# Performance work log

Hardware: AMD Instinct MI355X
Metric: run time of the kernel (lower is better)

## Reference

```python
import jax, jax.numpy as jnp
import numpy as np

B, T, E = 4, 2048, 1024
H, D = 8, 128  # num_query_heads, head_dimension (single shared KV head -> MQA)


def sinusoidal_pe(length, dim, dtype=jnp.float32):
    """Standard additive sinusoidal PE table of shape (length, dim)."""
    pos = jnp.arange(length, dtype=jnp.float32)[:, None]            # (L, 1)
    inv_freq = jnp.exp(-jnp.log(jnp.float32(10000.0)) * (jnp.arange(0, dim, 2, dtype=jnp.float32) / dim))
    ang = pos * inv_freq[None, :]                                    # (L, dim//2)
    pe = jnp.zeros((length, dim), dtype=jnp.float32)
    pe = pe.at[:, 0::2].set(jnp.sin(ang)).at[:, 1::2].set(jnp.cos(ang))
    return pe.astype(dtype)


def setup_inputs() -> dict:
    key = jax.random.key(0)
    kx, kq, kk, kv, ko = jax.random.split(key, 5)
    s = 0.02  # weight init scale
    return {
        "x": jax.random.normal(kx, (B, T, E), dtype=jnp.float32),
        "Wq": jax.random.normal(kq, (H * D, E), dtype=jnp.float32) * s,
        "Wk": jax.random.normal(kk, (D, E), dtype=jnp.float32) * s,
        "Wv": jax.random.normal(kv, (D, E), dtype=jnp.float32) * s,
        "Wo": jax.random.normal(ko, (E, H * D), dtype=jnp.float32) * s,
    }


def reference(x, Wq, Wk, Wv, Wo):
    Bv, Tv, Ev = x.shape
    scale = 1.0 / jnp.sqrt(jnp.float32(D)).astype(x.dtype)

    q = (x @ Wq.T).reshape(Bv, Tv, H, D)        # (B, T, H, D)
    k = (x @ Wk.T).reshape(Bv, Tv, 1, D)        # (B, T, 1, D) single KV head
    v = (x @ Wv.T).reshape(Bv, Tv, 1, D)

    # positional_embedding applied along axis -2 (as in (.., seq, dim) layout):
    # for k (B,T,1,D) the -2 axis has length 1 -> adds pe[0];
    # for q after permute (B,H,T,D) the -2 axis is T -> full table.
    k = k + sinusoidal_pe(1, D, k.dtype)        # broadcast over (B, T)

    q = jnp.transpose(q, (0, 2, 1, 3))          # (B, H, T, D)
    k1 = k[:, :, 0, :]                          # (B, T, D) shared KV head
    v1 = v[:, :, 0, :]                          # (B, T, D)

    q = q + sinusoidal_pe(Tv, D, q.dtype)[None, None]

    # MQA SDPA: broadcast single K/V head across H query heads
    scores = jnp.einsum("bhtd,bsd->bhts", q, k1) * scale   # (B, H, T, T)
    causal = jnp.tril(jnp.ones((Tv, Tv), dtype=bool))
    scores = jnp.where(causal[None, None], scores, jnp.finfo(scores.dtype).min)
    probs = jax.nn.softmax(scores, axis=-1)
    attn = jnp.einsum("bhts,bsd->bhtd", probs, v1)          # (B, H, T, D)

    out = jnp.transpose(attn, (0, 2, 1, 3)).reshape(Bv, Tv, H * D)
    return out @ Wo.T                                        # (B, T, E)
```

## Files before the change

### kernel.cpp

```cpp
#include <hip/hip_runtime.h>
#include <hip/hip_bf16.h>
#include <cstdint>
#include <cstddef>

#define B_ 4
#define T_ 2048
#define E_ 1024
#define H_ 8
#define D_ 128

typedef unsigned short u16;
typedef __bf16 bf16x8 __attribute__((ext_vector_type(8)));
typedef float f32x4 __attribute__((ext_vector_type(4)));

#define MFMA16(a, b, c) __builtin_amdgcn_mfma_f32_16x16x32_bf16((a), (b), (c), 0, 0, 0)

#if defined(__has_builtin)
#if __has_builtin(__builtin_amdgcn_global_load_lds)
#define HAVE_GLL 1
#endif
#if __has_builtin(__builtin_amdgcn_exp2f)
#define HAVE_EXP2 1
#endif
#endif

__device__ __forceinline__ void gload_lds16(const u16* g, u16* l) {
#ifdef HAVE_GLL
  __builtin_amdgcn_global_load_lds(
      (const __attribute__((address_space(1))) void*)g,
      (__attribute__((address_space(3))) void*)l, 16, 0, 0);
#else
  int lane = threadIdx.x & 63;
  *(uint4*)(l + lane * 8) = *(const uint4*)(g);
#endif
}

__device__ __forceinline__ float fexp2(float x) {
#ifdef HAVE_EXP2
  return __builtin_amdgcn_exp2f(x);
#else
  return __expf(x * 0.69314718056f);
#endif
}

__device__ __forceinline__ u16 f2bf(float f) {
  union { float f; uint32_t u; } a; a.f = f;
  uint32_t u = a.u;
  uint32_t r = (u + 0x7fffu + ((u >> 16) & 1u)) >> 16;
  return (u16)r;
}

__device__ __forceinline__ uint32_t pkbf(float lo, float hi) {
  uint32_t r;
  asm volatile("v_cvt_pk_bf16_f32 %0, %1, %2" : "=v"(r) : "v"(lo), "v"(hi));
  return r;
}

__device__ __forceinline__ void cvt4(const float* __restrict__ s, u16* __restrict__ d, int i4) {
  float4 v = *(const float4*)(s + (size_t)i4 * 4);
  uint2 o;
  o.x = (uint32_t)f2bf(v.x) | ((uint32_t)f2bf(v.y) << 16);
  o.y = (uint32_t)f2bf(v.z) | ((uint32_t)f2bf(v.w) << 16);
  *(uint2*)(d + (size_t)i4 * 4) = o;
}

__global__ __launch_bounds__(256) void prep_kernel(
    const float* __restrict__ x,  const float* __restrict__ Wq,
    const float* __restrict__ Wk, const float* __restrict__ Wv,
    const float* __restrict__ Wo,
    u16* __restrict__ xbf, u16* __restrict__ Wcat, u16* __restrict__ Wobf,
    float* __restrict__ pe)
{
  int id = blockIdx.x * 256 + threadIdx.x;
  if (id < 2097152) { cvt4(x, xbf, id); return; }
  id -= 2097152;
  if (id < 262144) { cvt4(Wq, Wcat, id); return; }
  id -= 262144;
  if (id < 32768) { cvt4(Wk, Wcat + 1048576, id); return; }
  id -= 32768;
  if (id < 32768) { cvt4(Wv, Wcat + 1179648, id); return; }
  id -= 32768;
  if (id < 262144) { cvt4(Wo, Wobf, id); return; }
  id -= 262144;
  int t = id >> 6, i = id & 63;
  float f = expf(-logf(10000.0f) * (float)i / 64.0f);
  float ang = (float)t * f;
  pe[t * 128 + 2 * i]     = sinf(ang);
  pe[t * 128 + 2 * i + 1] = cosf(ang);
}

template<int MODE>
__global__ __launch_bounds__(256) void gemm_nt(
    const u16* __restrict__ A, const u16* __restrict__ Bm,
    u16* __restrict__ Qb, u16* __restrict__ Kb, u16* __restrict__ VTb,
    const float* __restrict__ pe, float* __restrict__ Cout, int K)
{
  __shared__ u16 Al[128 * 32];
  __shared__ u16 Bl[128 * 32];
  const int t = threadIdx.x;
  const int l = t & 63, w = t >> 6;
  const int wr = w >> 1, wc = w & 1;
  const int bm = blockIdx.x * 128, bn = blockIdx.y * 128;
  const int lr = l & 15, lg = l >> 4;

  const int srow = w * 32 + (l >> 2);
  const int scol = (l & 3) * 8;
  const u16* gA0 = A + (size_t)(bm + srow) * K + scol;
  const u16* gB0 = Bm + (size_t)(bn + srow) * K + scol;
  u16* lA0 = &Al[(w * 32) * 32];
  u16* lA1 = &Al[(w * 32 + 16) * 32];
  u16* lB0 = &Bl[(w * 32) * 32];
  u16* lB1 = &Bl[(w * 32 + 16) * 32];
  const size_t r16 = (size_t)16 * K;

  f32x4 acc[4][4] = {};

  for (int k0 = 0; k0 < K; k0 += 32) {
    gload_lds16(gA0 + k0, lA0);
    gload_lds16(gA0 + r16 + k0, lA1);
    gload_lds16(gB0 + k0, lB0);
    gload_lds16(gB0 + r16 + k0, lB1);
    __syncthreads();
    bf16x8 af[4], bfr[4];
    #pragma unroll
    for (int m = 0; m < 4; ++m)
      af[m] = *(const bf16x8*)(&Al[(wr * 64 + m * 16 + lr) * 32 + lg * 8]);
    #pragma unroll
    for (int n = 0; n < 4; ++n)
      bfr[n] = *(const bf16x8*)(&Bl[(wc * 64 + n * 16 + lr) * 32 + lg * 8]);
    __builtin_amdgcn_s_setprio(1);
    #pragma unroll
    for (int m = 0; m < 4; ++m) {
      #pragma unroll
      for (int n = 0; n < 4; ++n)
        acc[m][n] = MFMA16(af[m], bfr[n], acc[m][n]);
    }
    __builtin_amdgcn_s_setprio(0);
    __syncthreads();
  }

  const float qscale = 0.12752869468f;
  #pragma unroll
  for (int m = 0; m < 4; ++m) {
    #pragma unroll
    for (int n = 0; n < 4; ++n) {
      const int gm0 = bm + wr * 64 + m * 16 + lg * 4;
      const int gn = bn + wc * 64 + n * 16 + lr;
      if constexpr (MODE == 0) {
        const int b = gm0 >> 11, tq0 = gm0 & (T_ - 1);
        if (gn < 1024) {
          int hh = gn >> 7, d = gn & 127;
          #pragma unroll
          for (int r = 0; r < 4; ++r)
            Qb[(((size_t)(b * H_ + hh) * T_ + tq0 + r) << 7) + d] =
                f2bf((acc[m][n][r] + pe[((tq0 + r) << 7) + d]) * qscale);
        } else if (gn < 1152) {
          int d = gn - 1024;
          #pragma unroll
          for (int r = 0; r < 4; ++r)
            Kb[((size_t)(gm0 + r) << 7) + d] = f2bf(acc[m][n][r] + (float)(d & 1));
        } else {
          int d = gn - 1152;
          uint2 pk;
          pk.x = pkbf(acc[m][n][0], acc[m][n][1]);
          pk.y = pkbf(acc[m][n][2], acc[m][n][3]);
          *(uint2*)(VTb + ((size_t)(b * 128 + d) << 11) + tq0) = pk;
        }
      } else {
        #pragma unroll
        for (int r = 0; r < 4; ++r)
          Cout[(size_t)(gm0 + r) * 1024 + gn] = acc[m][n][r];
      }
    }
  }
}

__global__ __launch_bounds__(512) void attn_kernel(
    const u16* __restrict__ Qb, const u16* __restrict__ Kb,
    const u16* __restrict__ VTg, u16* __restrict__ Ob)
{
  __shared__ u16 Kl[2][128 * 128];
  __shared__ u16 VTl[2][128 * 128];
  __shared__ u16 Pl[8 * 16 * 64];
  const int t = threadIdx.x;
  const int l = t & 63, w = t >> 6;
  const int lr = l & 15, lg = l >> 4;
  const int sw = lr & 7;
  const int p = blockIdx.x, b = blockIdx.y;
  const int h = w;
  const int q0A = p * 16, q0B = (127 - p) * 16;
  const int ntA = (q0A + 16 + 127) >> 7, ntB = (q0B + 16 + 127) >> 7;

  auto stage = [&](int kt, int s) {
    #pragma unroll
    for (int c = 0; c < 4; ++c) {
      int n = c * 512 + t;
      int row = n >> 4, ul = n & 15;
      int ug = ul ^ (row & 7);
      gload_lds16(Kb + ((size_t)(b * T_ + kt * 128 + row) << 7) + ug * 8,
                  &Kl[s][(size_t)(c * 512 + w * 64) * 8]);
      gload_lds16(VTg + ((size_t)(b * 128 + row) << 11) + kt * 128 + ug * 8,
                  &VTl[s][(size_t)(c * 512 + w * 64) * 8]);
    }
  };

  const u16* qbA = Qb + (((size_t)(b * H_ + h) * T_ + q0A + lr) << 7);
  const u16* qbB = Qb + (((size_t)(b * H_ + h) * T_ + q0B + lr) << 7);
  bf16x8 qfA[4], qfB[4];
  #pragma unroll
  for (int kc = 0; kc < 4; ++kc) {
    qfA[kc] = *(const bf16x8*)(qbA + kc * 32 + lg * 8);
    qfB[kc] = *(const bf16x8*)(qbB + kc * 32 + lg * 8);
  }

  float mA = -3e38f, mB = -3e38f, lA = 0.f, lB = 0.f;
  f32x4 oA[8] = {}, oB[8] = {};
  u16* pw = &Pl[w * 16 * 64];

  auto process = [&](f32x4 (&s)[8], float& m, float& lsum, f32x4 (&o)[8],
                     int q0F, int kt, bool masked, const u16* vtl) {
    float pv[32];
    float pm = -3e38f;
    if (masked) {
      const int qv = q0F + lr;
      #pragma unroll
      for (int kvf = 0; kvf < 8; ++kvf) {
        #pragma unroll
        for (int r = 0; r < 4; ++r) {
          int kv = kt * 128 + kvf * 16 + lg * 4 + r;
          float sv = (kv <= qv) ? s[kvf][r] : -3e38f;
          pv[kvf * 4 + r] = sv;
          pm = fmaxf(pm, sv);
        }
      }
    } else {
      #pragma unroll
      for (int kvf = 0; kvf < 8; ++kvf) {
        #pragma unroll
        for (int r = 0; r < 4; ++r) {
          float sv = s[kvf][r];
          pv[kvf * 4 + r] = sv;
          pm = fmaxf(pm, sv);
        }
      }
    }
    pm = fmaxf(pm, __shfl_xor(pm, 16));
    pm = fmaxf(pm, __shfl_xor(pm, 32));
    float mn;
    if (__all(pm <= m + 11.5f)) {
      mn = m;
    } else {
      mn = fmaxf(m, pm);
      float corr = fexp2(m - mn);
      lsum *= corr;
      #pragma unroll
      for (int df = 0; df < 8; ++df) {
        #pragma unroll
        for (int r = 0; r < 4; ++r) o[df][r] *= corr;
      }
      m = mn;
    }
    float ps = 0.f;
    #pragma unroll
    for (int i = 0; i < 32; ++i) {
      pv[i] = fexp2(pv[i] - mn);
      ps += pv[i];
    }
    ps += __shfl_xor(ps, 16);
    ps += __shfl_xor(ps, 32);
    lsum += ps;
    #pragma unroll
    for (int h2 = 0; h2 < 2; ++h2) {
      #pragma unroll
      for (int k4 = 0; k4 < 4; ++k4) {
        int kvf = h2 * 4 + k4;
        uint2 pk;
        pk.x = pkbf(pv[kvf * 4 + 0], pv[kvf * 4 + 1]);
        pk.y = pkbf(pv[kvf * 4 + 2], pv[kvf * 4 + 3]);
        int un = ((2 * k4 + (lg >> 1)) ^ sw) * 8 + (lg & 1) * 4;
        *(uint2*)(&pw[lr * 64 + un]) = pk;
      }
      __builtin_amdgcn_s_setprio(1);
      #pragma unroll
      for (int kc = 0; kc < 2; ++kc) {
        int kcg = h2 * 2 + kc;
        bf16x8 pf = *(const bf16x8*)(&pw[lr * 64 + ((4 * kc + lg) ^ sw) * 8]);
        #pragma unroll
        for (int df = 0; df < 8; ++df) {
          bf16x8 vf = *(const bf16x8*)(
              &vtl[((df * 16 + lr) << 7) + ((4 * kcg + lg) ^ sw) * 8]);
          o[df] = MFMA16(vf, pf, o[df]);
        }
      }
      __builtin_amdgcn_s_setprio(0);
    }
  };

  stage(0, 0);
  __syncthreads();

  for (int kt = 0; kt < ntB; ++kt) {
    const int cur = kt & 1;
    if (kt + 1 < ntB) stage(kt + 1, cur ^ 1);

    const bool actA = kt < ntA;
    f32x4 sA[8] = {}, sB[8] = {};
    __builtin_amdgcn_s_setprio(1);
    #pragma unroll
    for (int kvf = 0; kvf < 8; ++kvf) {
      bf16x8 kf[4];
      #pragma unroll
      for (int kc = 0; kc < 4; ++kc)
        kf[kc] = *(const bf16x8*)(
            &Kl[cur][((kvf * 16 + lr) << 7) + ((4 * kc + lg) ^ sw) * 8]);
      #pragma unroll
      for (int kc = 0; kc < 4; ++kc)
        sB[kvf] = MFMA16(kf[kc], qfB[kc], sB[kvf]);
      if (actA) {
        #pragma unroll
        for (int kc = 0; kc < 4; ++kc)
          sA[kvf] = MFMA16(kf[kc], qfA[kc], sA[kvf]);
      }
    }
    __builtin_amdgcn_s_setprio(0);
    process(sB, mB, lB, oB, q0B, kt, kt * 128 + 127 > q0B, &VTl[cur][0]);
    if (actA) process(sA, mA, lA, oA, q0A, kt, kt * 128 + 127 > q0A, &VTl[cur][0]);
    __syncthreads();
  }

  float rA = 1.0f / lA, rB = 1.0f / lB;
  #pragma unroll
  for (int df = 0; df < 8; ++df) {
    uint2 pk;
    pk.x = pkbf(oB[df][0] * rB, oB[df][1] * rB);
    pk.y = pkbf(oB[df][2] * rB, oB[df][3] * rB);
    *(uint2*)(Ob + ((size_t)(b * T_ + q0B + lr) << 10) + h * 128 + df * 16 + lg * 4) = pk;
    pk.x = pkbf(oA[df][0] * rA, oA[df][1] * rA);
    pk.y = pkbf(oA[df][2] * rA, oA[df][3] * rA);
    *(uint2*)(Ob + ((size_t)(b * T_ + q0A + lr) << 10) + h * 128 + df * 16 + lg * 4) = pk;
  }
}

extern "C" void kernel_launch(void* const* d_in, const int* in_sizes, int n_in,
                              void* d_out, int out_size, void* d_ws, size_t ws_size,
                              hipStream_t stream) {
  const float* x  = (const float*)d_in[0];
  const float* Wq = (const float*)d_in[1];
  const float* Wk = (const float*)d_in[2];
  const float* Wv = (const float*)d_in[3];
  const float* Wo = (const float*)d_in[4];

  char* ws = (char*)d_ws;
  size_t off = 0;
  auto alloc = [&](size_t bytes) {
    char* p = ws + off;
    off += (bytes + 255) & ~(size_t)255;
    return p;
  };
  u16*   xbf  = (u16*)  alloc(8388608ull * 2);
  u16*   Wcat = (u16*)  alloc(1310720ull * 2);
  u16*   Wobf = (u16*)  alloc(1048576ull * 2);
  float* pe   = (float*)alloc(262144ull * 4);
  u16*   Qbuf = (u16*)  alloc(8388608ull * 2);
  u16*   Kbuf = (u16*)  alloc(1048576ull * 2);
  u16*   VTbuf= (u16*)  alloc(1048576ull * 2);
  u16*   Abuf = (u16*)  alloc(8388608ull * 2);

  prep_kernel<<<11008, 256, 0, stream>>>(x, Wq, Wk, Wv, Wo, xbf, Wcat, Wobf, pe);

  gemm_nt<0><<<dim3(64, 10), 256, 0, stream>>>(xbf, Wcat, Qbuf, Kbuf, VTbuf, pe, nullptr, 1024);
  attn_kernel<<<dim3(64, 4), 512, 0, stream>>>(Qbuf, Kbuf, VTbuf, Abuf);
  gemm_nt<1><<<dim3(64, 8), 256, 0, stream>>>(Abuf, Wobf, nullptr, nullptr, nullptr, nullptr,
                                              (float*)d_out, 1024);
}
```

Before: 143.5 us.

## Double GEMM K-tile to 64 with XOR-swizzled LDS layout

The projection GEMM now stages a 128x64 K-slice of A and B per iteration instead of 128x32. This halves the number of barrier pairs and loop iterations over K. The LDS layout uses an XOR swizzle on the 16-byte chunk index so the fragment reads avoid bank conflicts with the wider 128-byte rows. It doubles shared memory per block, which may lower occupancy, and there is still no double buffering.

```diff
diff --git a/kernel.cpp b/kernel.cpp
--- a/kernel.cpp
+++ b/kernel.cpp
@@ -95,45 +95,45 @@
     u16* __restrict__ Qb, u16* __restrict__ Kb, u16* __restrict__ VTb,
     const float* __restrict__ pe, float* __restrict__ Cout, int K)
 {
-  __shared__ u16 Al[128 * 32];
-  __shared__ u16 Bl[128 * 32];
+  __shared__ u16 Al[128 * 64];
+  __shared__ u16 Bl[128 * 64];
   const int t = threadIdx.x;
   const int l = t & 63, w = t >> 6;
   const int wr = w >> 1, wc = w & 1;
   const int bm = blockIdx.x * 128, bn = blockIdx.y * 128;
   const int lr = l & 15, lg = l >> 4;
-
-  const int srow = w * 32 + (l >> 2);
-  const int scol = (l & 3) * 8;
-  const u16* gA0 = A + (size_t)(bm + srow) * K + scol;
-  const u16* gB0 = Bm + (size_t)(bn + srow) * K + scol;
-  u16* lA0 = &Al[(w * 32) * 32];
-  u16* lA1 = &Al[(w * 32 + 16) * 32];
-  u16* lB0 = &Bl[(w * 32) * 32];
-  u16* lB1 = &Bl[(w * 32 + 16) * 32];
-  const size_t r16 = (size_t)16 * K;
+  const int sw = lr & 7;
 
   f32x4 acc[4][4] = {};
 
-  for (int k0 = 0; k0 < K; k0 += 32) {
-    gload_lds16(gA0 + k0, lA0);
-    gload_lds16(gA0 + r16 + k0, lA1);
-    gload_lds16(gB0 + k0, lB0);
-    gload_lds16(gB0 + r16 + k0, lB1);
+  for (int k0 = 0; k0 < K; k0 += 64) {
+    #pragma unroll
+    for (int c = 0; c < 4; ++c) {
+      int n = c * 256 + t;
+      int row = n >> 3, ul = n & 7;
+      int ug = ul ^ (row & 7);
+      gload_lds16(A + (size_t)(bm + row) * K + k0 + ug * 8,
+                  &Al[(size_t)(c * 256 + w * 64) * 8]);
+      gload_lds16(Bm + (size_t)(bn + row) * K + k0 + ug * 8,
+                  &Bl[(size_t)(c * 256 + w * 64) * 8]);
+    }
     __syncthreads();
-    bf16x8 af[4], bfr[4];
-    #pragma unroll
-    for (int m = 0; m < 4; ++m)
-      af[m] = *(const bf16x8*)(&Al[(wr * 64 + m * 16 + lr) * 32 + lg * 8]);
-    #pragma unroll
-    for (int n = 0; n < 4; ++n)
-      bfr[n] = *(const bf16x8*)(&Bl[(wc * 64 + n * 16 + lr) * 32 + lg * 8]);
     __builtin_amdgcn_s_setprio(1);
     #pragma unroll
-    for (int m = 0; m < 4; ++m) {
+    for (int kk = 0; kk < 2; ++kk) {
+      bf16x8 af[4], bfr[4];
+      #pragma unroll
+      for (int m = 0; m < 4; ++m)
+        af[m] = *(const bf16x8*)(&Al[(wr * 64 + m * 16 + lr) * 64 + ((kk * 4 + lg) ^ sw) * 8]);
       #pragma unroll
       for (int n = 0; n < 4; ++n)
-        acc[m][n] = MFMA16(af[m], bfr[n], acc[m][n]);
+        bfr[n] = *(const bf16x8*)(&Bl[(wc * 64 + n * 16 + lr) * 64 + ((kk * 4 + lg) ^ sw) * 8]);
+      #pragma unroll
+      for (int m = 0; m < 4; ++m) {
+        #pragma unroll
+        for (int n = 0; n < 4; ++n)
+          acc[m][n] = MFMA16(af[m], bfr[n], acc[m][n]);
+      }
     }
     __builtin_amdgcn_s_setprio(0);
     __syncthreads();
```

Measured after the change: 146.4 us. No clear change (+2.0%).
